# Optimization experiments

Measured on AMD Instinct MI355X. Metric: run time of the kernel, lower is better.

The kernel has to match this reference:

```python
import jax, jax.numpy as jnp
import numpy as np

D_MODEL = 1024
N_HEADS = 16
CHUNK = 64
EPS = 1e-6


def elu_plus_1(x):
    return jax.nn.elu(x) + 1.0


def setup_inputs() -> dict:
    key = jax.random.key(0)
    kx, kq, kk, kv, ko = jax.random.split(key, 5)
    B, T = 4, 4096
    # xavier_uniform for square (D, D) weights: limit = sqrt(6/(D+D))
    lim = float(np.sqrt(6.0 / (D_MODEL + D_MODEL)))
    mk = lambda k: jax.random.uniform(k, (D_MODEL, D_MODEL), jnp.float32, -lim, lim)
    return {
        "x": jax.random.normal(kx, (B, T, D_MODEL), jnp.float32),
        "W_q": mk(kq),
        "W_k": mk(kk),
        "W_v": mk(kv),
        "W_o": mk(ko),
    }


def reference(x, W_q, W_k, W_v, W_o):
    B, T, D = x.shape
    H = N_HEADS
    dk = D // H
    dv = dk
    C = CHUNK
    N = T // C  # T chosen divisible by chunk size (no padding needed)

    q = (x @ W_q.T).reshape(B, T, H, dk)
    k = (x @ W_k.T).reshape(B, T, H, dk)
    v = (x @ W_v.T).reshape(B, T, H, dv)

    phi_q = elu_plus_1(q).reshape(B, N, C, H, dk)
    phi_k = elu_plus_1(k).reshape(B, N, C, H, dk)
    vc = v.reshape(B, N, C, H, dv)

    # Per-chunk key-value outer products and key sums, then exclusive prefix
    # sums over chunks give the carried state S and normalizer z at each
    # chunk's start (same math as the sequential chunk loop).
    KV = jnp.einsum('bnchk,bnchv->bnhkv', phi_k, vc)      # (B,N,H,dk,dv)
    Ksum = phi_k.sum(axis=2)                               # (B,N,C->sum,H,dk) -> (B,N,H,dk)
    KV_cum = jnp.cumsum(KV, axis=1)
    Ksum_cum = jnp.cumsum(Ksum, axis=1)
    S_prefix = jnp.concatenate([jnp.zeros_like(KV_cum[:, :1]), KV_cum[:, :-1]], axis=1)
    z_prefix = jnp.concatenate([jnp.zeros_like(Ksum_cum[:, :1]), Ksum_cum[:, :-1]], axis=1)

    # Inter-chunk contribution from carried state
    inter = jnp.einsum('bnchk,bnhkv->bnchv', phi_q, S_prefix)   # (B,N,C,H,dv)
    z_inter = jnp.einsum('bnchk,bnhk->bnch', phi_q, z_prefix)   # (B,N,C,H)

    # Intra-chunk causal attention
    mask = jnp.tril(jnp.ones((C, C), dtype=x.dtype))
    attn = jnp.einsum('bnihk,bnjhk->bnhij', phi_q, phi_k) * mask  # (B,N,H,C,C)
    intra = jnp.einsum('bnhij,bnjhv->bnihv', attn, vc)            # (B,N,C,H,dv)
    z_intra = attn.sum(axis=-1).transpose(0, 1, 3, 2)             # (B,N,C,H)

    denom = jnp.clip((z_inter + z_intra)[..., None], 1e-6, None)
    y = (inter + intra) / denom                                   # (B,N,C,H,dv)
    y = y.reshape(B, T, H * dv)
    return y @ W_o.T
```

## Files before the change

kernel.cpp:

```cpp
#include <hip/hip_runtime.h>


typedef unsigned short u16;
typedef float  f32x4 __attribute__((ext_vector_type(4)));
typedef short  b16x8 __attribute__((ext_vector_type(8)));
typedef u16    u16x4 __attribute__((ext_vector_type(4)));
typedef u16    u16x8 __attribute__((ext_vector_type(8)));

#define DEVINL __device__ __forceinline__

DEVINL u16 f2b(float f) {
  unsigned u = __float_as_uint(f);
  return (u16)((u + 0x7fffu + ((u >> 16) & 1u)) >> 16);
}
DEVINL float b2f(u16 s) { return __uint_as_float(((unsigned)s) << 16); }

DEVINL f32x4 mfma16(b16x8 a, b16x8 b, f32x4 c) {
  return __builtin_amdgcn_mfma_f32_16x16x32_bf16(a, b, c, 0, 0, 0);
}

DEVINL float phi_elu1(float v) { return v > 0.f ? v + 1.f : __expf(v); }

__global__ void cvt_all(const float* __restrict__ x,
                        const float* __restrict__ Wq, const float* __restrict__ Wk,
                        const float* __restrict__ Wv, const float* __restrict__ Wo,
                        u16* __restrict__ xb, u16* __restrict__ wqb,
                        u16* __restrict__ wkb, u16* __restrict__ wvb,
                        u16* __restrict__ wob) {
  const float* in;
  u16* out;
  int blk0, nblk, n8;
  const int b = blockIdx.x;
  if (b < 2048) {
    in = x; out = xb; blk0 = b; nblk = 2048; n8 = 2097152;
  } else {
    const int w = (b - 2048) >> 7;
    blk0 = (b - 2048) & 127; nblk = 128; n8 = 131072;
    switch (w) {
      case 0: in = Wq; out = wqb; break;
      case 1: in = Wk; out = wkb; break;
      case 2: in = Wv; out = wvb; break;
      default: in = Wo; out = wob; break;
    }
  }
  const int stride = nblk * 256;
  for (int i = blk0 * 256 + threadIdx.x; i < n8; i += stride) {
    const float* p = in + (size_t)i * 8;
    f32x4 a = *(const f32x4*)p;
    f32x4 c = *(const f32x4*)(p + 4);
    u16x8 o;
    o[0] = f2b(a[0]); o[1] = f2b(a[1]); o[2] = f2b(a[2]); o[3] = f2b(a[3]);
    o[4] = f2b(c[0]); o[5] = f2b(c[1]); o[6] = f2b(c[2]); o[7] = f2b(c[3]);
    *(u16x8*)(out + (size_t)i * 8) = o;
  }
}

#define STAGE(tt, h)                                                            \
  do {                                                                          \
    const u16* s_ = ((h) < 2 ? sA : sB) + (size_t)(((h) & 1) * 128) * 1024 +    \
                    (size_t)(tt) * 64;                                          \
    char* d_ = ldsStage + (((tt) & 1) << 16) + ((h) < 2 ? 0 : 32768) +          \
               (((h) & 1) << 14);                                               \
    __builtin_amdgcn_global_load_lds(                                           \
        (const __attribute__((address_space(1))) void*)(s_),                    \
        (__attribute__((address_space(3))) void*)(d_), 16, 0, 0);               \
    __builtin_amdgcn_global_load_lds(                                           \
        (const __attribute__((address_space(1))) void*)(s_ + 64 * 1024),        \
        (__attribute__((address_space(3))) void*)(d_ + 8192), 16, 0, 0);        \
  } while (0)

#define BAR_SB()                                                                \
  do {                                                                          \
    __builtin_amdgcn_s_barrier();                                               \
    __builtin_amdgcn_sched_barrier(0);                                          \
  } while (0)

template <bool PHI, typename OT>
__global__ __launch_bounds__(512, 2) void gemm256g(const u16* __restrict__ A,
                                                   const u16* __restrict__ B,
                                                   OT* __restrict__ C, int M, int N) {
  __shared__ char lds[131072];
  const int tid = threadIdx.x, wid = tid >> 6, l = tid & 63;
  const int l15 = l & 15, lg = l >> 4;
  const int wr = wid >> 2, wc = wid & 3;
  const int ntn = N >> 8;
  const int nwg = gridDim.x, bid = blockIdx.x;
  const int cpx = nwg >> 3;
  const int sb = (bid & 7) * cpx + (bid >> 3);
  const int tm = sb / ntn, tn = sb - tm * ntn;
  const int colX0 = (lg * 16) ^ ((l15 & 7) << 4);
  const int colX1 = (64 + lg * 16) ^ ((l15 & 7) << 4);
  char* ldsA = lds + wr * 16384 + l15 * 128;
  char* ldsB = lds + 32768 + (wc >> 1) * 16384 + ((wc & 1) * 64 + l15) * 128;
  const int srow = tid >> 3;
  const int scol = ((((tid & 7) * 16) ^ ((srow & 7) << 4)) >> 1);
  const u16* sA = A + (size_t)(tm * 256 + srow) * 1024 + scol;
  const u16* sB = B + (size_t)(tn * 256 + srow) * 1024 + scol;
  char* ldsStage = lds + wid * 1024;

  f32x4 acc[8][4];
#pragma unroll
  for (int i = 0; i < 8; i++)
#pragma unroll
    for (int j = 0; j < 4; j++) acc[i][j] = f32x4{0.f, 0.f, 0.f, 0.f};

  STAGE(0, 0); STAGE(0, 1); STAGE(0, 2); STAGE(0, 3);
  STAGE(1, 2); STAGE(1, 3);
  asm volatile("s_waitcnt vmcnt(4)" ::: "memory");

  b16x8 a0[4], a1[4], b0[4], b1[4];
  for (int t = 0; t < 16; ++t) {
    const int cb = (t & 1) << 16;
    BAR_SB();
#pragma unroll
    for (int fm = 0; fm < 4; fm++) {
      a0[fm] = *(const b16x8*)(ldsA + cb + fm * 2048 + colX0);
      a1[fm] = *(const b16x8*)(ldsA + cb + (4 + fm) * 2048 + colX0);
    }
#pragma unroll
    for (int fn = 0; fn < 4; fn++) b0[fn] = *(const b16x8*)(ldsB + cb + fn * 2048 + colX0);
    if (t < 15) { STAGE(t + 1, 0); STAGE(t + 1, 1); }
    __builtin_amdgcn_s_setprio(1);
#pragma unroll
    for (int fm = 0; fm < 4; fm++)
#pragma unroll
      for (int fn = 0; fn < 4; fn++) {
        acc[fm][fn] = mfma16(a0[fm], b0[fn], acc[fm][fn]);
        acc[4 + fm][fn] = mfma16(a1[fm], b0[fn], acc[4 + fm][fn]);
      }
    __builtin_amdgcn_s_setprio(0);
    BAR_SB();
#pragma unroll
    for (int fm = 0; fm < 4; fm++) {
      a0[fm] = *(const b16x8*)(ldsA + cb + fm * 2048 + colX1);
      a1[fm] = *(const b16x8*)(ldsA + cb + (4 + fm) * 2048 + colX1);
    }
#pragma unroll
    for (int fn = 0; fn < 4; fn++) b1[fn] = *(const b16x8*)(ldsB + cb + fn * 2048 + colX1);
    if (t < 14) { STAGE(t + 2, 2); STAGE(t + 2, 3); }
    __builtin_amdgcn_s_setprio(1);
#pragma unroll
    for (int fm = 0; fm < 4; fm++)
#pragma unroll
      for (int fn = 0; fn < 4; fn++) {
        acc[fm][fn] = mfma16(a0[fm], b1[fn], acc[fm][fn]);
        acc[4 + fm][fn] = mfma16(a1[fm], b1[fn], acc[4 + fm][fn]);
      }
    __builtin_amdgcn_s_setprio(0);
    if (t < 14) asm volatile("s_waitcnt vmcnt(4)" ::: "memory");
    else        asm volatile("s_waitcnt vmcnt(0)" ::: "memory");
  }

#pragma unroll
  for (int fm = 0; fm < 8; ++fm)
#pragma unroll
    for (int fn = 0; fn < 4; ++fn)
#pragma unroll
      for (int r = 0; r < 4; ++r) {
        size_t grow = (size_t)tm * 256 + wr * 128 + fm * 16 + lg * 4 + r;
        size_t gcol = (size_t)tn * 256 + wc * 64 + fn * 16 + l15;
        float v = acc[fm][fn][r];
        if (PHI) v = phi_elu1(v);
        OT* p = C + grow * (size_t)N + gcol;
        if constexpr (sizeof(OT) == 2) *p = (OT)f2b(v);
        else                           *p = (OT)v;
      }
}

__global__ __launch_bounds__(256, 2) void kv_kernel(const u16* __restrict__ phiK,
                                                    const u16* __restrict__ vT,
                                                    u16* __restrict__ KVT,
                                                    float* __restrict__ Ksum) {
  __shared__ u16 tile[4][64][68];
  const int tid = threadIdx.x, wid = tid >> 6, l = tid & 63, l15 = l & 15, lg = l >> 4;
  const int bid = blockIdx.x, hg = bid & 3, bn = bid >> 2, n = bn & 63, b = bn >> 6;
  const int h = hg * 4 + wid;
  const size_t row0 = (size_t)b * 4096 + n * 64;
  const int dcol = h * 64;
  const size_t cb = (size_t)b * 4096 + n * 64 + lg * 8;

  b16x8 af[4][2];
#pragma unroll
  for (int fm = 0; fm < 4; fm++)
#pragma unroll
    for (int ks = 0; ks < 2; ks++)
      af[fm][ks] = *(const b16x8*)(vT + (size_t)(h * 64 + fm * 16 + l15) * 16384 + cb + ks * 32);

  u16 (*tw)[68] = tile[wid];
#pragma unroll
  for (int i = 0; i < 8; i++) {
    int tok = i * 8 + (l >> 3);
    int c8 = (l & 7) * 8;
    u16x8 v = *(const u16x8*)(phiK + (row0 + tok) * 1024 + dcol + c8);
    *(u16x4*)(&tw[tok][c8]) = u16x4{v[0], v[1], v[2], v[3]};
    *(u16x4*)(&tw[tok][c8 + 4]) = u16x4{v[4], v[5], v[6], v[7]};
  }
  __syncthreads();

  b16x8 bf[4][2];
#pragma unroll
  for (int fn = 0; fn < 4; fn++)
#pragma unroll
    for (int ks = 0; ks < 2; ks++) {
      b16x8 t;
#pragma unroll
      for (int j = 0; j < 8; j++)
        t[j] = (short)tw[lg * 8 + ks * 32 + j][fn * 16 + l15];
      bf[fn][ks] = t;
    }

  f32x4 acc[4][4];
#pragma unroll
  for (int i = 0; i < 4; i++)
#pragma unroll
    for (int j = 0; j < 4; j++) acc[i][j] = f32x4{0.f, 0.f, 0.f, 0.f};
#pragma unroll
  for (int ks = 0; ks < 2; ks++)
#pragma unroll
    for (int fm = 0; fm < 4; fm++)
#pragma unroll
      for (int fn = 0; fn < 4; fn++) acc[fm][fn] = mfma16(af[fm][ks], bf[fn][ks], acc[fm][fn]);

  float ksum[4] = {0.f, 0.f, 0.f, 0.f};
#pragma unroll
  for (int fn = 0; fn < 4; fn++) {
#pragma unroll
    for (int ks = 0; ks < 2; ks++)
#pragma unroll
      for (int j = 0; j < 8; j++) ksum[fn] += b2f((u16)bf[fn][ks][j]);
    ksum[fn] += __shfl_xor(ksum[fn], 16);
    ksum[fn] += __shfl_xor(ksum[fn], 32);
  }
  const size_t ob = (size_t)(b * 16 + h) * 64 + n;
  if (l < 16) {
#pragma unroll
    for (int fn = 0; fn < 4; fn++) Ksum[ob * 64 + fn * 16 + l15] = ksum[fn];
  }
#pragma unroll
  for (int fm = 0; fm < 4; fm++)
#pragma unroll
    for (int fn = 0; fn < 4; fn++)
#pragma unroll
      for (int r = 0; r < 4; r++)
        KVT[ob * 4096 + (size_t)(fm * 16 + lg * 4 + r) * 64 + fn * 16 + l15] =
            f2b(acc[fm][fn][r]);
}

__global__ __launch_bounds__(256) void scan_s(const u16* __restrict__ KVT,
                                              u16* __restrict__ ST,
                                              const float* __restrict__ Ksum,
                                              float* __restrict__ zpre) {
  if (blockIdx.x >= 1024) {
    const int gi = (blockIdx.x - 1024) * 256 + threadIdx.x;
    const size_t bh = gi >> 6;
    const int dk = gi & 63;
    float acc = 0.f;
    for (int n = 0; n < 64; n++) {
      size_t idx = (bh * 64 + n) * 64 + dk;
      zpre[idx] = acc;
      acc += Ksum[idx];
    }
    return;
  }
  const size_t base = (size_t)(blockIdx.x >> 4) * 64 * 4096 +
                      (blockIdx.x & 15) * 256 + threadIdx.x;
  float acc = 0.f;
  float v[4], w[4];
#pragma unroll
  for (int i = 0; i < 4; i++) v[i] = b2f(KVT[base + (size_t)i * 4096]);
  for (int n = 0; n < 64; n += 4) {
    if (n < 60) {
#pragma unroll
      for (int i = 0; i < 4; i++) w[i] = b2f(KVT[base + (size_t)(n + 4 + i) * 4096]);
    } else {
#pragma unroll
      for (int i = 0; i < 4; i++) w[i] = 0.f;
    }
#pragma unroll
    for (int i = 0; i < 4; i++) {
      ST[base + (size_t)(n + i) * 4096] = f2b(acc);
      acc += v[i];
    }
#pragma unroll
    for (int i = 0; i < 4; i++) v[i] = w[i];
  }
}

__global__ __launch_bounds__(256, 2) void attn_out(const u16* __restrict__ phiQ,
                                                   const u16* __restrict__ phiK,
                                                   const u16* __restrict__ vT,
                                                   const u16* __restrict__ ST,
                                                   const float* __restrict__ zpre,
                                                   u16* __restrict__ Y) {
  __shared__ char lds[4 * 8192 + 4 * 256];
  const int tid = threadIdx.x, wid = tid >> 6, l = tid & 63, l15 = l & 15, lg = l >> 4;
  const int bid = blockIdx.x, hg = bid & 3, bn = bid >> 2, n = bn & 63, b = bn >> 6;
  const int h = hg * 4 + wid;
  const size_t row0 = (size_t)b * 4096 + n * 64;
  const int dcol = h * 64;

  b16x8 qf[4][2];
#pragma unroll
  for (int fi = 0; fi < 4; fi++)
#pragma unroll
    for (int ks = 0; ks < 2; ks++)
      qf[fi][ks] = *(const b16x8*)(phiQ + (row0 + fi * 16 + l15) * 1024 + dcol + lg * 8 + ks * 32);

  f32x4 accT[4][4];
#pragma unroll
  for (int i = 0; i < 4; i++)
#pragma unroll
    for (int j = 0; j < 4; j++) accT[i][j] = f32x4{0.f, 0.f, 0.f, 0.f};
  {
    b16x8 kf[4][2];
#pragma unroll
    for (int fj = 0; fj < 4; fj++)
#pragma unroll
      for (int ks = 0; ks < 2; ks++)
        kf[fj][ks] = *(const b16x8*)(phiK + (row0 + fj * 16 + l15) * 1024 + dcol + lg * 8 + ks * 32);
#pragma unroll
    for (int ks = 0; ks < 2; ks++)
#pragma unroll
      for (int fj = 0; fj < 4; fj++)
#pragma unroll
        for (int fi = 0; fi < 4; fi++)
          accT[fj][fi] = mfma16(kf[fj][ks], qf[fi][ks], accT[fj][fi]);
  }

  const size_t zb = ((size_t)(b * 16 + h) * 64 + n) * 64;
  float zi[4] = {0.f, 0.f, 0.f, 0.f};
#pragma unroll
  for (int ks = 0; ks < 2; ks++) {
    f32x4 z0 = *(const f32x4*)(zpre + zb + lg * 8 + ks * 32);
    f32x4 z1 = *(const f32x4*)(zpre + zb + lg * 8 + ks * 32 + 4);
#pragma unroll
    for (int fi = 0; fi < 4; fi++)
#pragma unroll
      for (int j = 0; j < 4; j++) {
        zi[fi] += b2f((u16)qf[fi][ks][j])     * z0[j];
        zi[fi] += b2f((u16)qf[fi][ks][j + 4]) * z1[j];
      }
  }

  char* abuf = lds + wid * 8192;
  float zt[4] = {0.f, 0.f, 0.f, 0.f};
#pragma unroll
  for (int fi = 0; fi < 4; fi++) {
    const int i = fi * 16 + l15;
    const int swz = (i & 7) << 4;
#pragma unroll
    for (int fj = 0; fj < 4; fj++) {
      f32x4 v = accT[fj][fi];
#pragma unroll
      for (int r = 0; r < 4; r++) {
        int j = fj * 16 + lg * 4 + r;
        if (j > i) v[r] = 0.f;
        zt[fi] += v[r];
      }
      unsigned w0 = (unsigned)f2b(v[0]) | ((unsigned)f2b(v[1]) << 16);
      unsigned w1 = (unsigned)f2b(v[2]) | ((unsigned)f2b(v[3]) << 16);
      int jb = (fj * 16 + lg * 4) * 2;
      *(unsigned*)(abuf + i * 128 + (jb ^ swz)) = w0;
      *(unsigned*)(abuf + i * 128 + ((jb + 4) ^ swz)) = w1;
    }
  }

  float* dbuf = (float*)(lds + 32768 + wid * 256);
#pragma unroll
  for (int fi = 0; fi < 4; fi++) {
    float z = zi[fi] + zt[fi];
    z += __shfl_xor(z, 16);
    z += __shfl_xor(z, 32);
    float rd = 1.f / fmaxf(z, 1e-6f);
    if (l < 16) dbuf[fi * 16 + l15] = rd;
  }
  __syncthreads();

  b16x8 stf[4][2], vf[4][2];
  const size_t stb = ((size_t)(b * 16 + h) * 64 + n) * 4096;
#pragma unroll
  for (int fn = 0; fn < 4; fn++)
#pragma unroll
    for (int ks = 0; ks < 2; ks++) {
      stf[fn][ks] = *(const b16x8*)(ST + stb + (size_t)(fn * 16 + l15) * 64 + lg * 8 + ks * 32);
      vf[fn][ks]  = *(const b16x8*)(vT + (size_t)(dcol + fn * 16 + l15) * 16384 +
                                    (size_t)b * 4096 + n * 64 + lg * 8 + ks * 32);
    }
  f32x4 acc[4][4];
#pragma unroll
  for (int i = 0; i < 4; i++)
#pragma unroll
    for (int j = 0; j < 4; j++) acc[i][j] = f32x4{0.f, 0.f, 0.f, 0.f};
#pragma unroll
  for (int ks = 0; ks < 2; ks++)
#pragma unroll
    for (int fm = 0; fm < 4; fm++)
#pragma unroll
      for (int fn = 0; fn < 4; fn++) acc[fm][fn] = mfma16(qf[fm][ks], stf[fn][ks], acc[fm][fn]);
#pragma unroll
  for (int fm = 0; fm < 4; fm++) {
    const int i = fm * 16 + l15;
    const int swz = (i & 7) << 4;
#pragma unroll
    for (int ks = 0; ks < 2; ks++) {
      b16x8 af = *(const b16x8*)(abuf + i * 128 + ((ks * 64 + lg * 16) ^ swz));
#pragma unroll
      for (int fn = 0; fn < 4; fn++) acc[fm][fn] = mfma16(af, vf[fn][ks], acc[fm][fn]);
    }
  }

#pragma unroll
  for (int fm = 0; fm < 4; fm++)
#pragma unroll
    for (int r = 0; r < 4; r++) {
      float rd = dbuf[fm * 16 + lg * 4 + r];
#pragma unroll
      for (int fn = 0; fn < 4; fn++)
        Y[(row0 + fm * 16 + lg * 4 + r) * 1024 + dcol + fn * 16 + l15] =
            f2b(acc[fm][fn][r] * rd);
    }
}

extern "C" void kernel_launch(void* const* d_in, const int* in_sizes, int n_in,
                              void* d_out, int out_size, void* d_ws, size_t ws_size,
                              hipStream_t stream) {
  const float* x  = (const float*)d_in[0];
  const float* Wq = (const float*)d_in[1];
  const float* Wk = (const float*)d_in[2];
  const float* Wv = (const float*)d_in[3];
  const float* Wo = (const float*)d_in[4];
  float* out = (float*)d_out;

  char* ws = (char*)d_ws;
  size_t off = 0;
  auto alloc = [&](size_t bytes) -> char* {
    char* p = ws + off;
    off += (bytes + 255) & ~(size_t)255;
    return p;
  };
  u16*   xb   = (u16*)alloc(33554432);
  u16*   wqb  = (u16*)alloc(2097152);
  u16*   wkb  = (u16*)alloc(2097152);
  u16*   wvb  = (u16*)alloc(2097152);
  u16*   wob  = (u16*)alloc(2097152);
  u16*   phiQ = (u16*)alloc(33554432);
  u16*   phiK = (u16*)alloc(33554432);
  u16*   vT   = (u16*)alloc(33554432);
  u16*   KVT  = (u16*)alloc(33554432);
  float* Ksum = (float*)alloc(1048576);
  u16*   ST   = (u16*)alloc(33554432);
  float* zpre = (float*)alloc(1048576);
  u16*   y    = xb;

  cvt_all<<<2560, 256, 0, stream>>>(x, Wq, Wk, Wv, Wo, xb, wqb, wkb, wvb, wob);

  gemm256g<true, u16><<<256, 512, 0, stream>>>(xb, wqb, phiQ, 16384, 1024);
  gemm256g<true, u16><<<256, 512, 0, stream>>>(xb, wkb, phiK, 16384, 1024);
  gemm256g<false, u16><<<256, 512, 0, stream>>>(wvb, xb, vT, 1024, 16384);

  kv_kernel<<<1024, 256, 0, stream>>>(phiK, vT, KVT, Ksum);
  scan_s<<<1040, 256, 0, stream>>>(KVT, ST, Ksum, zpre);
  attn_out<<<1024, 256, 0, stream>>>(phiQ, phiK, vT, ST, zpre, y);

  gemm256g<false, float><<<256, 512, 0, stream>>>(y, wob, out, 16384, 1024);
}
```

Before: 229.6 us.

## Add 128x128-tile GEMM for Q projection and vectorize prefix scan to 32-bit

Adds a gemm128 kernel with 128x128 tiles, 256 threads and a double-buffered global-to-LDS pipeline, and uses it for the Q projection. The grid grows from 256 to 1024 workgroups, giving better CU occupancy and load balance at the cost of less data reuse per tile. Separately, the KV prefix scan now handles two bf16 values per thread through 32-bit loads and stores, which halves the scan grid and reduces memory instruction count. Only the Q projection is switched; the K, V and output GEMMs stay on the 256 kernel.

```diff
diff --git a/kernel.cpp b/kernel.cpp
--- a/kernel.cpp
+++ b/kernel.cpp
@@ -55,25 +55,16 @@
   }
 }
 
-#define STAGE(tt, h)                                                            \
-  do {                                                                          \
-    const u16* s_ = ((h) < 2 ? sA : sB) + (size_t)(((h) & 1) * 128) * 1024 +    \
-                    (size_t)(tt) * 64;                                          \
-    char* d_ = ldsStage + (((tt) & 1) << 16) + ((h) < 2 ? 0 : 32768) +          \
-               (((h) & 1) << 14);                                               \
-    __builtin_amdgcn_global_load_lds(                                           \
-        (const __attribute__((address_space(1))) void*)(s_),                    \
-        (__attribute__((address_space(3))) void*)(d_), 16, 0, 0);               \
-    __builtin_amdgcn_global_load_lds(                                           \
-        (const __attribute__((address_space(1))) void*)(s_ + 64 * 1024),        \
-        (__attribute__((address_space(3))) void*)(d_ + 8192), 16, 0, 0);        \
-  } while (0)
-
 #define BAR_SB()                                                                \
   do {                                                                          \
     __builtin_amdgcn_s_barrier();                                               \
     __builtin_amdgcn_sched_barrier(0);                                          \
   } while (0)
+
+#define GLOAD(s_, d_)                                                           \
+  __builtin_amdgcn_global_load_lds(                                             \
+      (const __attribute__((address_space(1))) void*)(s_),                      \
+      (__attribute__((address_space(3))) void*)(d_), 16, 0, 0)
 
 template <bool PHI, typename OT>
 __global__ __launch_bounds__(512, 2) void gemm256g(const u16* __restrict__ A,
@@ -98,6 +89,16 @@
   const u16* sB = B + (size_t)(tn * 256 + srow) * 1024 + scol;
   char* ldsStage = lds + wid * 1024;
 
+#define STAGE(tt, h)                                                            \
+  do {                                                                          \
+    const u16* s_ = ((h) < 2 ? sA : sB) + (size_t)(((h) & 1) * 128) * 1024 +    \
+                    (size_t)(tt) * 64;                                          \
+    char* d_ = ldsStage + (((tt) & 1) << 16) + ((h) < 2 ? 0 : 32768) +          \
+               (((h) & 1) << 14);                                               \
+    GLOAD(s_, d_);                                                              \
+    GLOAD(s_ + 64 * 1024, d_ + 8192);                                           \
+  } while (0)
+
   f32x4 acc[8][4];
 #pragma unroll
   for (int i = 0; i < 8; i++)
@@ -150,6 +151,7 @@
     if (t < 14) asm volatile("s_waitcnt vmcnt(4)" ::: "memory");
     else        asm volatile("s_waitcnt vmcnt(0)" ::: "memory");
   }
+#undef STAGE
 
 #pragma unroll
   for (int fm = 0; fm < 8; ++fm)
@@ -159,6 +161,97 @@
       for (int r = 0; r < 4; ++r) {
         size_t grow = (size_t)tm * 256 + wr * 128 + fm * 16 + lg * 4 + r;
         size_t gcol = (size_t)tn * 256 + wc * 64 + fn * 16 + l15;
+        float v = acc[fm][fn][r];
+        if (PHI) v = phi_elu1(v);
+        OT* p = C + grow * (size_t)N + gcol;
+        if constexpr (sizeof(OT) == 2) *p = (OT)f2b(v);
+        else                           *p = (OT)v;
+      }
+}
+
+template <bool PHI, typename OT>
+__global__ __launch_bounds__(256, 2) void gemm128(const u16* __restrict__ A,
+                                                  const u16* __restrict__ B,
+                                                  OT* __restrict__ C, int M, int N) {
+  __shared__ char lds[65536];
+  const int tid = threadIdx.x, wid = tid >> 6, l = tid & 63;
+  const int l15 = l & 15, lg = l >> 4;
+  const int wr = wid >> 1, wc = wid & 1;
+  const int ntn = N >> 7;
+  const int nwg = gridDim.x, bid = blockIdx.x;
+  const int cpx = nwg >> 3;
+  const int sb = (bid & 7) * cpx + (bid >> 3);
+  const int tm = sb / ntn, tn = sb - tm * ntn;
+  const int colX0 = (lg * 16) ^ ((l15 & 7) << 4);
+  const int colX1 = (64 + lg * 16) ^ ((l15 & 7) << 4);
+  char* ldsA = lds + (wr * 64 + l15) * 128;
+  char* ldsB = lds + 16384 + (wc * 64 + l15) * 128;
+  const int srow = tid >> 3;
+  const int scol = ((((tid & 7) * 16) ^ ((srow & 7) << 4)) >> 1);
+  const u16* sA = A + (size_t)(tm * 128 + srow) * 1024 + scol;
+  const u16* sB = B + (size_t)(tn * 128 + srow) * 1024 + scol;
+  char* ldsStage = lds + wid * 1024;
+
+#define STAGE(tt, h)                                                            \
+  do {                                                                          \
+    const u16* s_ = ((h) < 2 ? sA : sB) + (size_t)(((h) & 1) * 64) * 1024 +     \
+                    (size_t)(tt) * 64;                                          \
+    char* d_ = ldsStage + (((tt) & 1) << 15) + ((h) < 2 ? 0 : 16384) +          \
+               (((h) & 1) << 13);                                               \
+    GLOAD(s_, d_);                                                              \
+    GLOAD(s_ + 32 * 1024, d_ + 4096);                                           \
+  } while (0)
+
+  f32x4 acc[4][4];
+#pragma unroll
+  for (int i = 0; i < 4; i++)
+#pragma unroll
+    for (int j = 0; j < 4; j++) acc[i][j] = f32x4{0.f, 0.f, 0.f, 0.f};
+
+  STAGE(0, 0); STAGE(0, 1); STAGE(0, 2); STAGE(0, 3);
+  STAGE(1, 2); STAGE(1, 3);
+  asm volatile("s_waitcnt vmcnt(4)" ::: "memory");
+
+  b16x8 af[4], bf[4];
+  for (int t = 0; t < 16; ++t) {
+    const int cb = (t & 1) << 15;
+    BAR_SB();
+#pragma unroll
+    for (int fm = 0; fm < 4; fm++) af[fm] = *(const b16x8*)(ldsA + cb + fm * 2048 + colX0);
+#pragma unroll
+    for (int fn = 0; fn < 4; fn++) bf[fn] = *(const b16x8*)(ldsB + cb + fn * 2048 + colX0);
+    if (t < 15) { STAGE(t + 1, 0); STAGE(t + 1, 1); }
+    __builtin_amdgcn_s_setprio(1);
+#pragma unroll
+    for (int fm = 0; fm < 4; fm++)
+#pragma unroll
+      for (int fn = 0; fn < 4; fn++) acc[fm][fn] = mfma16(af[fm], bf[fn], acc[fm][fn]);
+    __builtin_amdgcn_s_setprio(0);
+    BAR_SB();
+#pragma unroll
+    for (int fm = 0; fm < 4; fm++) af[fm] = *(const b16x8*)(ldsA + cb + fm * 2048 + colX1);
+#pragma unroll
+    for (int fn = 0; fn < 4; fn++) bf[fn] = *(const b16x8*)(ldsB + cb + fn * 2048 + colX1);
+    if (t < 14) { STAGE(t + 2, 2); STAGE(t + 2, 3); }
+    __builtin_amdgcn_s_setprio(1);
+#pragma unroll
+    for (int fm = 0; fm < 4; fm++)
+#pragma unroll
+      for (int fn = 0; fn < 4; fn++) acc[fm][fn] = mfma16(af[fm], bf[fn], acc[fm][fn]);
+    __builtin_amdgcn_s_setprio(0);
+    if (t < 14) asm volatile("s_waitcnt vmcnt(4)" ::: "memory");
+    else        asm volatile("s_waitcnt vmcnt(0)" ::: "memory");
+  }
+#undef STAGE
+
+#pragma unroll
+  for (int fm = 0; fm < 4; ++fm)
+#pragma unroll
+    for (int fn = 0; fn < 4; ++fn)
+#pragma unroll
+      for (int r = 0; r < 4; ++r) {
+        size_t grow = (size_t)tm * 128 + wr * 64 + fm * 16 + lg * 4 + r;
+        size_t gcol = (size_t)tn * 128 + wc * 64 + fn * 16 + l15;
         float v = acc[fm][fn][r];
         if (PHI) v = phi_elu1(v);
         OT* p = C + grow * (size_t)N + gcol;
@@ -250,8 +343,8 @@
                                               u16* __restrict__ ST,
                                               const float* __restrict__ Ksum,
                                               float* __restrict__ zpre) {
-  if (blockIdx.x >= 1024) {
-    const int gi = (blockIdx.x - 1024) * 256 + threadIdx.x;
+  if (blockIdx.x >= 512) {
+    const int gi = (blockIdx.x - 512) * 256 + threadIdx.x;
     const size_t bh = gi >> 6;
     const int dk = gi & 63;
     float acc = 0.f;
@@ -262,24 +355,28 @@
     }
     return;
   }
-  const size_t base = (size_t)(blockIdx.x >> 4) * 64 * 4096 +
-                      (blockIdx.x & 15) * 256 + threadIdx.x;
-  float acc = 0.f;
-  float v[4], w[4];
-#pragma unroll
-  for (int i = 0; i < 4; i++) v[i] = b2f(KVT[base + (size_t)i * 4096]);
+  const size_t base2 = (size_t)(blockIdx.x >> 3) * 64 * 2048 +
+                       (blockIdx.x & 7) * 256 + threadIdx.x;
+  const unsigned* KV32 = (const unsigned*)KVT;
+  unsigned* ST32 = (unsigned*)ST;
+  float ac0 = 0.f, ac1 = 0.f;
+  unsigned v[4], w[4];
+#pragma unroll
+  for (int i = 0; i < 4; i++) v[i] = KV32[base2 + (size_t)i * 2048];
   for (int n = 0; n < 64; n += 4) {
     if (n < 60) {
 #pragma unroll
-      for (int i = 0; i < 4; i++) w[i] = b2f(KVT[base + (size_t)(n + 4 + i) * 4096]);
+      for (int i = 0; i < 4; i++) w[i] = KV32[base2 + (size_t)(n + 4 + i) * 2048];
     } else {
 #pragma unroll
-      for (int i = 0; i < 4; i++) w[i] = 0.f;
+      for (int i = 0; i < 4; i++) w[i] = 0u;
     }
 #pragma unroll
     for (int i = 0; i < 4; i++) {
-      ST[base + (size_t)(n + i) * 4096] = f2b(acc);
-      acc += v[i];
+      ST32[base2 + (size_t)(n + i) * 2048] =
+          (unsigned)f2b(ac0) | ((unsigned)f2b(ac1) << 16);
+      ac0 += b2f((u16)(v[i] & 0xffff));
+      ac1 += b2f((u16)(v[i] >> 16));
     }
 #pragma unroll
     for (int i = 0; i < 4; i++) v[i] = w[i];
@@ -454,12 +551,12 @@
 
   cvt_all<<<2560, 256, 0, stream>>>(x, Wq, Wk, Wv, Wo, xb, wqb, wkb, wvb, wob);
 
-  gemm256g<true, u16><<<256, 512, 0, stream>>>(xb, wqb, phiQ, 16384, 1024);
+  gemm128<true, u16><<<1024, 256, 0, stream>>>(xb, wqb, phiQ, 16384, 1024);
   gemm256g<true, u16><<<256, 512, 0, stream>>>(xb, wkb, phiK, 16384, 1024);
   gemm256g<false, u16><<<256, 512, 0, stream>>>(wvb, xb, vT, 1024, 16384);
 
   kv_kernel<<<1024, 256, 0, stream>>>(phiK, vT, KVT, Ksum);
-  scan_s<<<1040, 256, 0, stream>>>(KVT, ST, Ksum, zpre);
+  scan_s<<<528, 256, 0, stream>>>(KVT, ST, Ksum, zpre);
   attn_out<<<1024, 256, 0, stream>>>(phiQ, phiK, vT, ST, zpre, y);
 
   gemm256g<false, float><<<256, 512, 0, stream>>>(y, wob, out, 16384, 1024);
```

Result: no change. 229.5 us (-0.1%).
